# Optimization experiments

Measured on AMD Instinct MI355X. Metric: run time of the kernel, lower is better.

The kernel has to match this reference:

```python
import jax, jax.numpy as jnp
import numpy as np


def setup_inputs() -> dict:
    key = jax.random.key(0)
    ks = jax.random.split(key, 8)
    N, E, F_IN, H, OUT = 20000, 320000, 386, 256, 2
    x = jax.random.normal(ks[0], (N, F_IN), dtype=jnp.float32)
    src = jax.random.randint(ks[1], (E,), 0, N)
    dst = jax.random.randint(ks[2], (E,), 0, N)
    W1 = jax.random.normal(ks[3], (F_IN, H), dtype=jnp.float32) / np.sqrt(F_IN)
    b1 = jnp.zeros((H,), dtype=jnp.float32)
    W2 = jax.random.normal(ks[4], (H, OUT), dtype=jnp.float32) / np.sqrt(H)
    b2 = jnp.zeros((OUT,), dtype=jnp.float32)
    return {"x": x, "src": src, "dst": dst, "W1": W1, "b1": b1, "W2": W2, "b2": b2}


def reference(x, src, dst, W1, b1, W2, b2):
    N = x.shape[0]
    # PyG GCNConv: add self-loops, deg from destination (col), sym normalization
    deg = jnp.ones((N,), x.dtype).at[dst].add(1.0)  # self-loop + in-degree
    dis = deg ** -0.5                                # deg^{-1/2}
    edge_norm = dis[src] * dis[dst]                  # [E]
    self_norm = dis * dis                            # [N] (self-loop weight)

    def gcn_conv(h, W, b):
        h = h @ W                                    # [N, F_out] transform first
        msgs = h[src] * edge_norm[:, None]           # [E, F_out] gathered messages
        agg = jax.ops.segment_sum(msgs, dst, num_segments=N)
        agg = agg + h * self_norm[:, None]           # self-loop contribution
        return agg + b

    h = jax.nn.relu(gcn_conv(x, W1, b1))
    out = gcn_conv(h, W2, b2)
    return jnp.tanh(out)
```

## Files before the change

### kernel.cpp

```cpp
#include <hip/hip_runtime.h>
#include <math.h>

typedef _Float16 f16;
typedef _Float16 f16x8 __attribute__((ext_vector_type(8)));
typedef float f32x4 __attribute__((ext_vector_type(4)));

#define FIN 386
#define KP  416
#define HH  256
#define ELLW 64
#define NP  20096

#define BTM 128
#define BTN 64
#define GBK 32


__global__ __launch_bounds__(256) void k_prep(
    int* __restrict__ cursor, int N,
    const float* __restrict__ W1, f16* __restrict__ wt,
    const float* __restrict__ x, f16* __restrict__ xh) {
    int i = blockIdx.x * 256 + threadIdx.x;
    if (i < N) cursor[i] = 0;
    if (i < HH * KP) {
        int c = i / KP, k = i - c * KP;
        wt[i] = (k < FIN) ? (f16)W1[(size_t)k * HH + c] : (f16)0.f;
    }
    const int CPR = KP / 8;
    if (i < NP * CPR) {
        int row = i / CPR;
        int k2 = (i - row * CPR) * 8;
        f16x8 t = {};
        if (row < N && k2 < FIN) {
            const float* p = x + (size_t)row * FIN + k2;
            if (k2 + 8 <= FIN) {
                float2 f0 = *(const float2*)(p);
                float2 f1 = *(const float2*)(p + 2);
                float2 f2 = *(const float2*)(p + 4);
                float2 f3 = *(const float2*)(p + 6);
                t[0] = (f16)f0.x; t[1] = (f16)f0.y;
                t[2] = (f16)f1.x; t[3] = (f16)f1.y;
                t[4] = (f16)f2.x; t[5] = (f16)f2.y;
                t[6] = (f16)f3.x; t[7] = (f16)f3.y;
            } else {
                #pragma unroll
                for (int j = 0; j < 8; ++j)
                    t[j] = (k2 + j < FIN) ? (f16)p[j] : (f16)0.f;
            }
        }
        *(f16x8*)(xh + (size_t)row * KP + k2) = t;
    }
}


__global__ __launch_bounds__(256) void k_mid(
    const f16* __restrict__ A, const f16* __restrict__ Bt,
    f16* __restrict__ C, int nbg,
    const int* __restrict__ src, const int* __restrict__ dst,
    int* __restrict__ cursor, int* __restrict__ ell, int E, int nbf) {
    __shared__ f16 Bs[BTN * KP];

    if ((int)blockIdx.x >= nbg) {
        for (int e = ((int)blockIdx.x - nbg) * 256 + threadIdx.x; e < E; e += nbf * 256) {
            int s = src[e], d = dst[e];
            int slot = atomicAdd(&cursor[d], 1);
            if (slot < ELLW) ell[(size_t)d * ELLW + slot] = s;
        }
        return;
    }

    const int gb = blockIdx.x;
    const int bm = (gb >> 2) * BTM;
    const int bn = (gb & 3) * BTN;
    const int tid = threadIdx.x;
    const int w = tid >> 6, l = tid & 63;
    const int lrow = l & 15, lslot = l >> 4;

    for (int c = tid; c < BTN * (KP / 8); c += 256) {
        int row = c / (KP / 8);
        int k8 = (c - row * (KP / 8)) * 8;
        *(f16x8*)&Bs[row * KP + k8] = *(const f16x8*)(Bt + (size_t)(bn + row) * KP + k8);
    }
    __syncthreads();

    const f16* pa0 = A + (size_t)(bm + w * 32 + lrow) * KP + lslot * 8;
    const f16* pa1 = pa0 + (size_t)16 * KP;

    f32x4 acc[2][4] = {};

    f16x8 a0c = *(const f16x8*)(pa0);
    f16x8 a1c = *(const f16x8*)(pa1);

    #pragma unroll
    for (int k0 = 0; k0 < KP; k0 += GBK) {
        f16x8 a0n = a0c, a1n = a1c;
        if (k0 + GBK < KP) {
            a0n = *(const f16x8*)(pa0 + k0 + GBK);
            a1n = *(const f16x8*)(pa1 + k0 + GBK);
        }
        #pragma unroll
        for (int ni = 0; ni < 4; ++ni) {
            f16x8 b = *(const f16x8*)&Bs[(ni * 16 + lrow) * KP + lslot * 8 + k0];
            acc[0][ni] = __builtin_amdgcn_mfma_f32_16x16x32_f16(a0c, b, acc[0][ni], 0, 0, 0);
            acc[1][ni] = __builtin_amdgcn_mfma_f32_16x16x32_f16(a1c, b, acc[1][ni], 0, 0, 0);
        }
        a0c = a0n; a1c = a1n;
    }

    #pragma unroll
    for (int mi = 0; mi < 2; ++mi) {
        #pragma unroll
        for (int r = 0; r < 4; ++r) {
            int row = bm + w * 32 + mi * 16 + lslot * 4 + r;
            #pragma unroll
            for (int ni = 0; ni < 4; ++ni)
                C[(size_t)row * HH + bn + ni * 16 + lrow] = (f16)acc[mi][ni][r];
        }
    }
}


__global__ __launch_bounds__(256) void k_agg1(
    const f16* __restrict__ h1h, const int* __restrict__ ell,
    const int* __restrict__ cursor, const float* __restrict__ b1,
    const float* __restrict__ W2, float* __restrict__ z, int N) {
    const int sl = threadIdx.x & 31;
    const int d = blockIdx.x * 8 + (threadIdx.x >> 5);
    if (d >= N) return;

    const float4* bp = (const float4*)b1 + sl * 2;
    const float4 bb0 = bp[0], bb1 = bp[1];
    const float4* wp = (const float4*)W2 + sl * 4;
    const float4 wv0 = wp[0], wv1 = wp[1], wv2 = wp[2], wv3 = wp[3];

    int cd = cursor[d];
    float dd = rsqrtf((float)(cd + 1));
    int cnt = cd > ELLW ? ELLW : cd;
    const int* erow = ell + (size_t)d * ELLW;

    f16x8 v = ((const f16x8*)(h1h + (size_t)d * HH))[sl];
    float e[8];
    #pragma unroll
    for (int i = 0; i < 8; ++i) e[i] = dd * (float)v[i];

    int j = 0;
    for (; j + 3 < cnt; j += 4) {
        int s0 = erow[j], s1 = erow[j + 1], s2 = erow[j + 2], s3 = erow[j + 3];
        float u0 = rsqrtf((float)(cursor[s0] + 1));
        float u1 = rsqrtf((float)(cursor[s1] + 1));
        float u2 = rsqrtf((float)(cursor[s2] + 1));
        float u3 = rsqrtf((float)(cursor[s3] + 1));
        f16x8 q0 = ((const f16x8*)(h1h + (size_t)s0 * HH))[sl];
        f16x8 q1 = ((const f16x8*)(h1h + (size_t)s1 * HH))[sl];
        f16x8 q2 = ((const f16x8*)(h1h + (size_t)s2 * HH))[sl];
        f16x8 q3 = ((const f16x8*)(h1h + (size_t)s3 * HH))[sl];
        #pragma unroll
        for (int i = 0; i < 8; ++i)
            e[i] += u0 * (float)q0[i] + u1 * (float)q1[i]
                  + u2 * (float)q2[i] + u3 * (float)q3[i];
    }
    for (; j < cnt; ++j) {
        int s0 = erow[j];
        float u0 = rsqrtf((float)(cursor[s0] + 1));
        f16x8 q0 = ((const f16x8*)(h1h + (size_t)s0 * HH))[sl];
        #pragma unroll
        for (int i = 0; i < 8; ++i) e[i] += u0 * (float)q0[i];
    }

    float a[8];
    a[0] = fmaxf(dd * e[0] + bb0.x, 0.0f);
    a[1] = fmaxf(dd * e[1] + bb0.y, 0.0f);
    a[2] = fmaxf(dd * e[2] + bb0.z, 0.0f);
    a[3] = fmaxf(dd * e[3] + bb0.w, 0.0f);
    a[4] = fmaxf(dd * e[4] + bb1.x, 0.0f);
    a[5] = fmaxf(dd * e[5] + bb1.y, 0.0f);
    a[6] = fmaxf(dd * e[6] + bb1.z, 0.0f);
    a[7] = fmaxf(dd * e[7] + bb1.w, 0.0f);

    float p0 = a[0] * wv0.x + a[1] * wv0.z + a[2] * wv1.x + a[3] * wv1.z
             + a[4] * wv2.x + a[5] * wv2.z + a[6] * wv3.x + a[7] * wv3.z;
    float p1 = a[0] * wv0.y + a[1] * wv0.w + a[2] * wv1.y + a[3] * wv1.w
             + a[4] * wv2.y + a[5] * wv2.w + a[6] * wv3.y + a[7] * wv3.w;
    #pragma unroll
    for (int off = 16; off > 0; off >>= 1) {
        p0 += __shfl_down(p0, off, 32);
        p1 += __shfl_down(p1, off, 32);
    }
    if (sl == 0)
        *(float2*)(z + 2 * (size_t)d) = make_float2(p0, p1);
}


__global__ __launch_bounds__(256) void k_agg2(
    const float* __restrict__ z, const int* __restrict__ ell,
    const int* __restrict__ cursor, const float* __restrict__ b2,
    float* __restrict__ out, int N) {
    int d = blockIdx.x * 256 + threadIdx.x;
    if (d >= N) return;
    const float c0 = b2[0], c1 = b2[1];
    int cd = cursor[d];
    float dd = rsqrtf((float)(cd + 1));
    int cnt = cd > ELLW ? ELLW : cd;
    const int* erow = ell + (size_t)d * ELLW;
    float2 zz = *(const float2*)(z + 2 * (size_t)d);
    float e0 = dd * zz.x, e1 = dd * zz.y;
    int j = 0;
    for (; j + 3 < cnt; j += 4) {
        int s0 = erow[j], s1 = erow[j + 1], s2 = erow[j + 2], s3 = erow[j + 3];
        float u0 = rsqrtf((float)(cursor[s0] + 1));
        float u1 = rsqrtf((float)(cursor[s1] + 1));
        float u2 = rsqrtf((float)(cursor[s2] + 1));
        float u3 = rsqrtf((float)(cursor[s3] + 1));
        float2 z0 = *(const float2*)(z + 2 * (size_t)s0);
        float2 z1 = *(const float2*)(z + 2 * (size_t)s1);
        float2 z2 = *(const float2*)(z + 2 * (size_t)s2);
        float2 z3 = *(const float2*)(z + 2 * (size_t)s3);
        e0 += u0 * z0.x + u1 * z1.x + u2 * z2.x + u3 * z3.x;
        e1 += u0 * z0.y + u1 * z1.y + u2 * z2.y + u3 * z3.y;
    }
    for (; j < cnt; ++j) {
        int s = erow[j];
        float u = rsqrtf((float)(cursor[s] + 1));
        float2 zv = *(const float2*)(z + 2 * (size_t)s);
        e0 += u * zv.x;
        e1 += u * zv.y;
    }
    out[d * 2 + 0] = tanhf(dd * e0 + c0);
    out[d * 2 + 1] = tanhf(dd * e1 + c1);
}


extern "C" void kernel_launch(void* const* d_in, const int* in_sizes, int n_in,
                              void* d_out, int out_size, void* d_ws, size_t ws_size,
                              hipStream_t stream) {
    const float* x   = (const float*)d_in[0];
    const int*   src = (const int*)d_in[1];
    const int*   dst = (const int*)d_in[2];
    const float* W1  = (const float*)d_in[3];
    const float* b1  = (const float*)d_in[4];
    const float* W2  = (const float*)d_in[5];
    const float* b2  = (const float*)d_in[6];
    float* out = (float*)d_out;

    const int E = in_sizes[1];
    const int N = in_sizes[0] / FIN;

    char* base = (char*)d_ws;
    size_t off = 0;
    f16* wt     = (f16*)(base + off); off += (size_t)HH * KP * sizeof(f16);
    f16* xh     = (f16*)(base + off); off += (size_t)NP * KP * sizeof(f16);
    f16* h1h    = (f16*)(base + off); off += (size_t)NP * HH * sizeof(f16);
    int* ell    = (int*)(base + off); off += (size_t)N * ELLW * sizeof(int);
    float* z    = (float*)(base + off); off += 2 * (size_t)N * sizeof(float);
    int* cursor = (int*)(base + off); off += (size_t)N * sizeof(int);

    const int T = 256;
    const int CPR = KP / 8;
    const int prep_work = NP * CPR;
    const int nbg = (NP / BTM) * (HH / BTN);
    const int nbf = 512;

    k_prep<<<(prep_work + T - 1) / T, T, 0, stream>>>(cursor, N, W1, wt, x, xh);
    k_mid<<<nbg + nbf, T, 0, stream>>>(xh, wt, h1h, nbg, src, dst, cursor, ell, E, nbf);
    k_agg1<<<(N + 7) / 8, T, 0, stream>>>(h1h, ell, cursor, b1, W2, z, N);
    k_agg2<<<(N + T - 1) / T, T, 0, stream>>>(z, ell, cursor, b2, out, N);
}
```

Measured before the change: 72.17 us.

## Hold W1 tile in registers instead of LDS and reorder fill blocks first

The GEMM tile width is halved and each wave now loads its W1 fragments straight from global memory into registers for the whole K range. This removes the shared-memory staging and the __syncthreads barrier, which frees LDS and should raise occupancy. The ELL-fill blocks are moved to the front of the grid so the atomic scatter starts early. In exchange, A is re-read by twice as many blocks and the register count per thread goes up (26 f16x8 B fragments per thread).

```diff
diff --git a/kernel.cpp b/kernel.cpp
--- a/kernel.cpp
+++ b/kernel.cpp
@@ -12,8 +12,9 @@
 #define NP  20096
 
 #define BTM 128
-#define BTN 64
+#define BTN 32
 #define GBK 32
+#define KSTEPS (KP / GBK)
 
 
 __global__ __launch_bounds__(256) void k_prep(
@@ -55,13 +56,12 @@
 
 __global__ __launch_bounds__(256) void k_mid(
     const f16* __restrict__ A, const f16* __restrict__ Bt,
-    f16* __restrict__ C, int nbg,
+    f16* __restrict__ C, int nbf,
     const int* __restrict__ src, const int* __restrict__ dst,
-    int* __restrict__ cursor, int* __restrict__ ell, int E, int nbf) {
-    __shared__ f16 Bs[BTN * KP];
-
-    if ((int)blockIdx.x >= nbg) {
-        for (int e = ((int)blockIdx.x - nbg) * 256 + threadIdx.x; e < E; e += nbf * 256) {
+    int* __restrict__ cursor, int* __restrict__ ell, int E) {
+
+    if ((int)blockIdx.x < nbf) {
+        for (int e = (int)blockIdx.x * 256 + threadIdx.x; e < E; e += nbf * 256) {
             int s = src[e], d = dst[e];
             int slot = atomicAdd(&cursor[d], 1);
             if (slot < ELLW) ell[(size_t)d * ELLW + slot] = s;
@@ -69,41 +69,40 @@
         return;
     }
 
-    const int gb = blockIdx.x;
-    const int bm = (gb >> 2) * BTM;
-    const int bn = (gb & 3) * BTN;
+    const int gb = (int)blockIdx.x - nbf;
+    const int bm = (gb >> 3) * BTM;
+    const int bn = (gb & 7) * BTN;
     const int tid = threadIdx.x;
     const int w = tid >> 6, l = tid & 63;
     const int lrow = l & 15, lslot = l >> 4;
 
-    for (int c = tid; c < BTN * (KP / 8); c += 256) {
-        int row = c / (KP / 8);
-        int k8 = (c - row * (KP / 8)) * 8;
-        *(f16x8*)&Bs[row * KP + k8] = *(const f16x8*)(Bt + (size_t)(bn + row) * KP + k8);
-    }
-    __syncthreads();
+    const f16* pb = Bt + (size_t)(bn + lrow) * KP + lslot * 8;
+    f16x8 breg[2][KSTEPS];
+    #pragma unroll
+    for (int ct = 0; ct < 2; ++ct)
+        #pragma unroll
+        for (int s = 0; s < KSTEPS; ++s)
+            breg[ct][s] = *(const f16x8*)(pb + (size_t)ct * 16 * KP + s * GBK);
 
     const f16* pa0 = A + (size_t)(bm + w * 32 + lrow) * KP + lslot * 8;
     const f16* pa1 = pa0 + (size_t)16 * KP;
 
-    f32x4 acc[2][4] = {};
+    f32x4 acc[2][2] = {};
 
     f16x8 a0c = *(const f16x8*)(pa0);
     f16x8 a1c = *(const f16x8*)(pa1);
 
     #pragma unroll
-    for (int k0 = 0; k0 < KP; k0 += GBK) {
+    for (int s = 0; s < KSTEPS; ++s) {
         f16x8 a0n = a0c, a1n = a1c;
-        if (k0 + GBK < KP) {
-            a0n = *(const f16x8*)(pa0 + k0 + GBK);
-            a1n = *(const f16x8*)(pa1 + k0 + GBK);
-        }
-        #pragma unroll
-        for (int ni = 0; ni < 4; ++ni) {
-            f16x8 b = *(const f16x8*)&Bs[(ni * 16 + lrow) * KP + lslot * 8 + k0];
-            acc[0][ni] = __builtin_amdgcn_mfma_f32_16x16x32_f16(a0c, b, acc[0][ni], 0, 0, 0);
-            acc[1][ni] = __builtin_amdgcn_mfma_f32_16x16x32_f16(a1c, b, acc[1][ni], 0, 0, 0);
-        }
+        if (s + 1 < KSTEPS) {
+            a0n = *(const f16x8*)(pa0 + (s + 1) * GBK);
+            a1n = *(const f16x8*)(pa1 + (s + 1) * GBK);
+        }
+        acc[0][0] = __builtin_amdgcn_mfma_f32_16x16x32_f16(a0c, breg[0][s], acc[0][0], 0, 0, 0);
+        acc[1][0] = __builtin_amdgcn_mfma_f32_16x16x32_f16(a1c, breg[0][s], acc[1][0], 0, 0, 0);
+        acc[0][1] = __builtin_amdgcn_mfma_f32_16x16x32_f16(a0c, breg[1][s], acc[0][1], 0, 0, 0);
+        acc[1][1] = __builtin_amdgcn_mfma_f32_16x16x32_f16(a1c, breg[1][s], acc[1][1], 0, 0, 0);
         a0c = a0n; a1c = a1n;
     }
 
@@ -113,8 +112,8 @@
         for (int r = 0; r < 4; ++r) {
             int row = bm + w * 32 + mi * 16 + lslot * 4 + r;
             #pragma unroll
-            for (int ni = 0; ni < 4; ++ni)
-                C[(size_t)row * HH + bn + ni * 16 + lrow] = (f16)acc[mi][ni][r];
+            for (int ct = 0; ct < 2; ++ct)
+                C[(size_t)row * HH + bn + ct * 16 + lrow] = (f16)acc[mi][ct][r];
         }
     }
 }
@@ -257,11 +256,11 @@
     const int T = 256;
     const int CPR = KP / 8;
     const int prep_work = NP * CPR;
+    const int nbf = 512;
     const int nbg = (NP / BTM) * (HH / BTN);
-    const int nbf = 512;
 
     k_prep<<<(prep_work + T - 1) / T, T, 0, stream>>>(cursor, N, W1, wt, x, xh);
-    k_mid<<<nbg + nbf, T, 0, stream>>>(xh, wt, h1h, nbg, src, dst, cursor, ell, E, nbf);
+    k_mid<<<nbf + nbg, T, 0, stream>>>(xh, wt, h1h, nbf, src, dst, cursor, ell, E);
     k_agg1<<<(N + 7) / 8, T, 0, stream>>>(h1h, ell, cursor, b1, W2, z, N);
     k_agg2<<<(N + T - 1) / T, T, 0, stream>>>(z, ell, cursor, b2, out, N);
 }
```

Result: slower. 91.27 us (+26.5%).
